# Kernel tuning notes

Measured on AMD Instinct MI355X. Metric: run time of the kernel, lower is better.

The kernel has to match this reference:

```python
import jax, jax.numpy as jnp
import numpy as np

NEG_SLOPE = 0.01  # torch LeakyReLU default

def setup_inputs() -> dict:
    key = jax.random.key(0)
    ks = jax.random.split(key, 8)
    B, T, D = 8, 2048, 512
    E, H = 8, 2 * D  # n_experts, ffn hidden
    s = 0.02
    return {
        "x":  jax.random.normal(ks[0], (B, T, D), dtype=jnp.float32),
        "Wr": jax.random.normal(ks[1], (D, E), dtype=jnp.float32) * s,
        "br": jnp.zeros((E,), dtype=jnp.float32),
        "W1": jax.random.normal(ks[2], (E, D, H), dtype=jnp.float32) * s,
        "b1": jnp.zeros((E, H), dtype=jnp.float32),
        "W2": jax.random.normal(ks[3], (E, H, D), dtype=jnp.float32) * s,
        "b2": jnp.zeros((E, D), dtype=jnp.float32),
    }

def reference(x, Wr, br, W1, b1, W2, b2):
    B, T, D = x.shape
    E = Wr.shape[1]
    top_k = 2
    balancing_coef = 1e-4
    x_flat = x.reshape(B * T, D)  # [N, D]

    # router: softmax over experts
    router_probs = jax.nn.softmax(x_flat @ Wr + br, axis=-1)  # [N, E]
    top_weights, top_indices = jax.lax.top_k(router_probs, top_k)  # [N, k]

    # dense all-expert FFN (faithful to original: every expert on every token)
    h = jax.nn.leaky_relu(jnp.einsum('nd,edh->neh', x_flat, W1) + b1, NEG_SLOPE)  # [N, E, H]
    expert_out = jax.nn.leaky_relu(jnp.einsum('neh,ehd->ned', h, W2) + b2, NEG_SLOPE)  # [N, E, D]
    # dropout is identity in eval mode

    # gather top-k expert outputs and combine with router weights
    top_out = jnp.take_along_axis(expert_out, top_indices[:, :, None], axis=1)  # [N, k, D]
    out_flat = jnp.sum(top_out * top_weights[:, :, None], axis=1)  # [N, D]
    output = out_flat.reshape(B, T, D)

    # load-balancing loss
    target = jnp.full((E,), 1.0 / E, dtype=x.dtype)
    mean_probs = jnp.mean(router_probs, axis=0)
    gating_loss = jnp.mean((target - mean_probs) ** 2) * balancing_coef
    return (output, gating_loss)
```

## Files before the change

kernel.cpp:

```cpp
#include <hip/hip_runtime.h>
#include <hip/hip_bf16.h>

constexpr int D_    = 512;
constexpr int H_    = 1024;
constexpr int E_    = 8;
constexpr int NTOK_ = 16384;
constexpr int MT_   = 64;
constexpr int NPAIR_= 2*NTOK_;
constexpr float NEG_ = 0.01f;

typedef short s16x8 __attribute__((ext_vector_type(8)));
typedef float f32x4 __attribute__((ext_vector_type(4)));

#define MFMA16(a,b,c) __builtin_amdgcn_mfma_f32_16x16x32_bf16((a),(b),(c),0,0,0)

__device__ __forceinline__ unsigned short f2bf(float f) {
  unsigned u = __float_as_uint(f);
  u += 0x7FFFu + ((u >> 16) & 1u);
  return (unsigned short)(u >> 16);
}
__device__ __forceinline__ float bf2f(unsigned u16) {
  return __uint_as_float(u16 << 16);
}
__device__ __forceinline__ float leaky(float v) {
  return v > 0.f ? v : NEG_ * v;
}

__global__ __launch_bounds__(256) void router_kernel(
    const float* __restrict__ x, const float* __restrict__ Wr,
    const float* __restrict__ br,
    int* __restrict__ cnt, float* __restrict__ psum,
    int* __restrict__ tokE, int* __restrict__ tokSlot, float* __restrict__ tokW) {
  const int blk = blockIdx.x;
  const int tid = threadIdx.x;
  __shared__ float SH[8256 + 32];
  const int t0 = blk * 64;
  float* xt   = SH;
  float* red  = SH;
  float* lp   = SH + 8256;
  int*  lcnt  = (int*)(SH + 8256 + 8);
  int*  gbase = (int*)(SH + 8256 + 16);
  if (tid < 8) { lcnt[tid] = 0; lp[tid] = 0.f; }

  const int tq = tid & 63;
  const int q  = tid >> 6;
  float acc[E_];
#pragma unroll
  for (int e = 0; e < E_; e++) acc[e] = 0.f;

  for (int c = 0; c < 4; c++) {
    __syncthreads();
#pragma unroll
    for (int it = 0; it < 8; it++) {
      int f = it * 256 + tid;
      int row = f >> 5, c4 = f & 31;
      float4 v = *(const float4*)(x + (size_t)(t0 + row) * D_ + c * 128 + c4 * 4);
      float* d = xt + row * 129 + c4 * 4;
      d[0] = v.x; d[1] = v.y; d[2] = v.z; d[3] = v.w;
    }
    __syncthreads();
#pragma unroll
    for (int j = 0; j < 32; j++) {
      float xv = xt[tq * 129 + q * 32 + j];
      const float* wr = Wr + (size_t)(c * 128 + q * 32 + j) * E_;
#pragma unroll
      for (int e = 0; e < E_; e++) acc[e] += xv * wr[e];
    }
  }
  __syncthreads();
#pragma unroll
  for (int e = 0; e < E_; e++) red[(q * 64 + tq) * 8 + e] = acc[e];
  __syncthreads();

  float m1 = -1.f, m2 = -1.f; int i1 = 0, i2 = 0, s1 = 0, s2 = 0;
  if (tid < 64) {
    float p[E_];
#pragma unroll
    for (int e = 0; e < E_; e++)
      p[e] = br[e] + red[tid * 8 + e] + red[(64 + tid) * 8 + e]
           + red[(128 + tid) * 8 + e] + red[(192 + tid) * 8 + e];
    float mx = p[0];
#pragma unroll
    for (int e = 1; e < E_; e++) mx = fmaxf(mx, p[e]);
    float s = 0.f;
#pragma unroll
    for (int e = 0; e < E_; e++) { p[e] = expf(p[e] - mx); s += p[e]; }
    float inv = 1.f / s;
#pragma unroll
    for (int e = 0; e < E_; e++) p[e] *= inv;

#pragma unroll
    for (int e = 0; e < E_; e++) {
      float pe = p[e];
      if (pe > m1)      { m2 = m1; i2 = i1; m1 = pe; i1 = e; }
      else if (pe > m2) { m2 = pe; i2 = e; }
    }
    s1 = atomicAdd(&lcnt[i1], 1);
    s2 = atomicAdd(&lcnt[i2], 1);
#pragma unroll
    for (int e = 0; e < E_; e++) atomicAdd(&lp[e], p[e]);
  }
  __syncthreads();
  if (tid < 8) {
    gbase[tid] = atomicAdd(&cnt[tid * 16], lcnt[tid]);
    atomicAdd(&psum[tid * 16], lp[tid]);
  }
  __syncthreads();
  if (tid < 64) {
    int gt = t0 + tid;
    tokE[2 * gt]     = i1; tokSlot[2 * gt]     = gbase[i1] + s1; tokW[2 * gt]     = m1;
    tokE[2 * gt + 1] = i2; tokSlot[2 * gt + 1] = gbase[i2] + s2; tokW[2 * gt + 1] = m2;
  }
}

__global__ __launch_bounds__(256) void convert_kernel(
    const float* __restrict__ W1, const float* __restrict__ W2,
    unsigned short* __restrict__ W1s, unsigned short* __restrict__ W2s) {
  __shared__ float ldsf[64 * 68];
  const int tid = threadIdx.x;
  int bid = blockIdx.x;
  const float* src;
  int eE, kt, tc, srcStride;
  bool isW1 = bid < 1024;
  if (isW1) {
    eE = bid >> 7; kt = (bid >> 4) & 7; tc = bid & 15; srcStride = 1024;
    src = W1 + ((size_t)(eE * 512 + kt * 64)) * 1024 + tc * 64;
  } else {
    int b2i = bid - 1024;
    eE = b2i >> 7; kt = (b2i >> 3) & 15; tc = b2i & 7; srcStride = 512;
    src = W2 + ((size_t)(eE * 1024 + kt * 64)) * 512 + tc * 64;
  }
#pragma unroll
  for (int rep = 0; rep < 4; rep++) {
    int row = rep * 16 + (tid >> 4);
    int c4  = (tid & 15) * 4;
    float4 v = *(const float4*)(src + (size_t)row * srcStride + c4);
    float* d = ldsf + row * 68 + c4;
    d[0] = v.x; d[1] = v.y; d[2] = v.z; d[3] = v.w;
  }
  __syncthreads();
  int wv = tid >> 6, lane = tid & 63;
#pragma unroll
  for (int qi = 0; qi < 2; qi++) {
    int qq = wv * 2 + qi;
    int ks = qq >> 2, nt = qq & 3;
    int k0 = ks * 32 + (lane >> 4) * 8;
    int n  = nt * 16 + (lane & 15);
    s16x8 v;
#pragma unroll
    for (int j = 0; j < 8; j++) v[j] = (short)f2bf(ldsf[(k0 + j) * 68 + n]);
    int ntg = tc * 4 + nt, kkg = kt * 2 + ks;
    if (isW1)
      *(s16x8*)(W1s + (((size_t)eE << 16) + (ntg << 10) + (kkg << 6) + lane) * 8) = v;
    else
      *(s16x8*)(W2s + (((size_t)eE << 16) + (ntg << 11) + (kkg << 6) + lane) * 8) = v;
  }
}

__global__ __launch_bounds__(256) void assign_kernel(
    const int* __restrict__ tokE, const int* __restrict__ tokSlot,
    const int* __restrict__ cnt, const float* __restrict__ psum,
    int* __restrict__ posOfTok, int* __restrict__ tokOfPos,
    float* __restrict__ loss_out) {
  __shared__ int soff[E_];
  int tid = threadIdx.x;
  if (tid == 0) {
    int o = 0;
#pragma unroll
    for (int e = 0; e < E_; e++) { soff[e] = o; o += cnt[e * 16]; }
  }
  __syncthreads();
  int p = blockIdx.x * 256 + tid;
  int pos = soff[tokE[p]] + tokSlot[p];
  posOfTok[p] = pos;
  tokOfPos[pos] = p >> 1;
  if (blockIdx.x == 0 && tid == 0) {
    float l = 0.f;
#pragma unroll
    for (int e = 0; e < E_; e++) {
      float d = 0.125f - psum[e * 16] / (float)NTOK_;
      l += d * d;
    }
    *loss_out = (l / 8.f) * 1e-4f;
  }
}

__global__ __launch_bounds__(512, 2) void ffn_kernel(
    const float* __restrict__ x,
    const unsigned short* __restrict__ W1s, const unsigned short* __restrict__ W2s,
    const float* __restrict__ b1, const float* __restrict__ b2,
    const int* __restrict__ cnt, const int* __restrict__ tokOfPos,
    unsigned short* __restrict__ buf) {
  const int e = blockIdx.x & 7;
  const int tile = blockIdx.x >> 3;
  int nTok = 0, base0 = 0;
#pragma unroll
  for (int i = 0; i < E_; i++) {
    int ci = cnt[i * 16];
    if (i < e) base0 += ci;
    if (i == e) nTok = ci;
  }
  const int start = tile * MT_;
  if (start >= nTok) return;
  const int valid = min(MT_, nTok - start);
  const int base = base0 + start;

  __shared__ __align__(16) unsigned short L[MT_][1032];

  const int tid = threadIdx.x;
  const int w = tid >> 6;
  const int lane = tid & 63;

  for (int r = w; r < MT_; r += 8) {
    int tok = tokOfPos[base + min(r, valid - 1)];
    const float4* src = (const float4*)(x + (size_t)tok * D_);
    float4 a = src[lane * 2], b = src[lane * 2 + 1];
    s16x8 v;
    v[0] = (short)f2bf(a.x); v[1] = (short)f2bf(a.y);
    v[2] = (short)f2bf(a.z); v[3] = (short)f2bf(a.w);
    v[4] = (short)f2bf(b.x); v[5] = (short)f2bf(b.y);
    v[6] = (short)f2bf(b.z); v[7] = (short)f2bf(b.w);
    *(s16x8*)&L[r][lane * 8] = v;
  }
  __syncthreads();

  const int qm = lane & 15;
  const int qk = (lane >> 4) * 8;
  const int qr = (lane >> 4) * 4;

  const unsigned short* A1 =
      W1s + (((size_t)e << 16) + ((size_t)(w * 8) << 10) + lane) * 8;
  f32x4 acc1[8][4];
#pragma unroll
  for (int mi = 0; mi < 8; mi++)
#pragma unroll
    for (int ni = 0; ni < 4; ni++) acc1[mi][ni] = {0.f, 0.f, 0.f, 0.f};

  s16x8 a1p[2][8];
#pragma unroll
  for (int s = 0; s < 2; s++)
#pragma unroll
    for (int mi = 0; mi < 8; mi++)
      a1p[s][mi] = *(const s16x8*)(A1 + (size_t)mi * 8192 + s * 512);

#pragma unroll
  for (int kk = 0; kk < 16; kk++) {
    s16x8 bcur[4];
#pragma unroll
    for (int ni = 0; ni < 4; ni++)
      bcur[ni] = *(const s16x8*)&L[ni * 16 + qm][kk * 32 + qk];
    __builtin_amdgcn_s_setprio(1);
#pragma unroll
    for (int mi = 0; mi < 8; mi++)
#pragma unroll
      for (int ni = 0; ni < 4; ni++)
        acc1[mi][ni] = MFMA16(a1p[kk & 1][mi], bcur[ni], acc1[mi][ni]);
    __builtin_amdgcn_s_setprio(0);
    if (kk + 2 < 16) {
#pragma unroll
      for (int mi = 0; mi < 8; mi++)
        a1p[kk & 1][mi] = *(const s16x8*)(A1 + (size_t)mi * 8192 + (kk + 2) * 512);
    }
  }
  __syncthreads();

  const unsigned short* A2 =
      W2s + (((size_t)e << 16) + ((size_t)(w * 4) << 11) + lane) * 8;
  s16x8 a2p[2][4];
#pragma unroll
  for (int s = 0; s < 2; s++)
#pragma unroll
    for (int mi = 0; mi < 4; mi++)
      a2p[s][mi] = *(const s16x8*)(A2 + (size_t)mi * 16384 + s * 512);

#pragma unroll
  for (int mi = 0; mi < 8; mi++) {
    int hb = w * 128 + mi * 16 + qr;
    float4 bv = *(const float4*)(b1 + (size_t)e * H_ + hb);
#pragma unroll
    for (int ni = 0; ni < 4; ni++) {
      int tr = ni * 16 + qm;
      ushort4 pk;
      pk.x = f2bf(leaky(acc1[mi][ni][0] + bv.x));
      pk.y = f2bf(leaky(acc1[mi][ni][1] + bv.y));
      pk.z = f2bf(leaky(acc1[mi][ni][2] + bv.z));
      pk.w = f2bf(leaky(acc1[mi][ni][3] + bv.w));
      *(ushort4*)&L[tr][hb] = pk;
    }
  }
  __syncthreads();

  f32x4 acc2[4][4];
#pragma unroll
  for (int mi = 0; mi < 4; mi++)
#pragma unroll
    for (int ni = 0; ni < 4; ni++) acc2[mi][ni] = {0.f, 0.f, 0.f, 0.f};

#pragma unroll
  for (int kk = 0; kk < 32; kk++) {
    s16x8 bcur[4];
#pragma unroll
    for (int ni = 0; ni < 4; ni++)
      bcur[ni] = *(const s16x8*)&L[ni * 16 + qm][kk * 32 + qk];
    __builtin_amdgcn_s_setprio(1);
#pragma unroll
    for (int mi = 0; mi < 4; mi++)
#pragma unroll
      for (int ni = 0; ni < 4; ni++)
        acc2[mi][ni] = MFMA16(a2p[kk & 1][mi], bcur[ni], acc2[mi][ni]);
    __builtin_amdgcn_s_setprio(0);
    if (kk + 2 < 32) {
#pragma unroll
      for (int mi = 0; mi < 4; mi++)
        a2p[kk & 1][mi] = *(const s16x8*)(A2 + (size_t)mi * 16384 + (kk + 2) * 512);
    }
  }

#pragma unroll
  for (int mi = 0; mi < 4; mi++) {
    int ob = w * 64 + mi * 16 + qr;
    float4 bv = *(const float4*)(b2 + (size_t)e * D_ + ob);
#pragma unroll
    for (int ni = 0; ni < 4; ni++) {
      int tok = ni * 16 + qm;
      if (tok < valid) {
        ushort4 pk;
        pk.x = f2bf(leaky(acc2[mi][ni][0] + bv.x));
        pk.y = f2bf(leaky(acc2[mi][ni][1] + bv.y));
        pk.z = f2bf(leaky(acc2[mi][ni][2] + bv.z));
        pk.w = f2bf(leaky(acc2[mi][ni][3] + bv.w));
        *(ushort4*)(buf + (size_t)(base + tok) * D_ + ob) = pk;
      }
    }
  }
}

__global__ __launch_bounds__(256) void combine_kernel(
    const unsigned short* __restrict__ buf, const int* __restrict__ posOfTok,
    const float* __restrict__ tokW, float* __restrict__ out) {
  int t = blockIdx.x * 4 + (threadIdx.x >> 6);
  int lane = threadIdx.x & 63;
  int p0 = posOfTok[2 * t], p1 = posOfTok[2 * t + 1];
  float w0 = tokW[2 * t], w1 = tokW[2 * t + 1];
  uint4 u0 = ((const uint4*)(buf + (size_t)p0 * D_))[lane];
  uint4 u1 = ((const uint4*)(buf + (size_t)p1 * D_))[lane];
  float4 oA, oB;
  oA.x = w0 * bf2f(u0.x & 0xFFFFu) + w1 * bf2f(u1.x & 0xFFFFu);
  oA.y = w0 * bf2f(u0.x >> 16)     + w1 * bf2f(u1.x >> 16);
  oA.z = w0 * bf2f(u0.y & 0xFFFFu) + w1 * bf2f(u1.y & 0xFFFFu);
  oA.w = w0 * bf2f(u0.y >> 16)     + w1 * bf2f(u1.y >> 16);
  oB.x = w0 * bf2f(u0.z & 0xFFFFu) + w1 * bf2f(u1.z & 0xFFFFu);
  oB.y = w0 * bf2f(u0.z >> 16)     + w1 * bf2f(u1.z >> 16);
  oB.z = w0 * bf2f(u0.w & 0xFFFFu) + w1 * bf2f(u1.w & 0xFFFFu);
  oB.w = w0 * bf2f(u0.w >> 16)     + w1 * bf2f(u1.w >> 16);
  float4* dst = (float4*)(out + (size_t)t * D_);
  dst[lane * 2]     = oA;
  dst[lane * 2 + 1] = oB;
}

extern "C" void kernel_launch(void* const* d_in, const int* in_sizes, int n_in,
                              void* d_out, int out_size, void* d_ws, size_t ws_size,
                              hipStream_t stream) {
  const float* x  = (const float*)d_in[0];
  const float* Wr = (const float*)d_in[1];
  const float* br = (const float*)d_in[2];
  const float* W1 = (const float*)d_in[3];
  const float* b1 = (const float*)d_in[4];
  const float* W2 = (const float*)d_in[5];
  const float* b2 = (const float*)d_in[6];
  float* out = (float*)d_out;

  char* ws = (char*)d_ws;
  int*   cnt      = (int*)(ws + 0);
  float* psum     = (float*)(ws + 512);
  int*   tokE     = (int*)(ws + 4096);
  int*   tokSlot  = (int*)(ws + 4096 + 1 * 131072);
  float* tokW     = (float*)(ws + 4096 + 2 * 131072);
  int*   posOfTok = (int*)(ws + 4096 + 3 * 131072);
  int*   tokOfPos = (int*)(ws + 4096 + 4 * 131072);
  unsigned short* W1s = (unsigned short*)(ws + (1u << 20));
  unsigned short* W2s = (unsigned short*)(ws + (1u << 20) + 16777216u);
  unsigned short* buf = (unsigned short*)(ws + (1u << 20) + 33554432u);

  hipMemsetAsync(d_ws, 0, 2048, stream);
  router_kernel<<<256, 256, 0, stream>>>(x, Wr, br, cnt, psum, tokE, tokSlot, tokW);
  convert_kernel<<<2048, 256, 0, stream>>>(W1, W2, W1s, W2s);
  assign_kernel<<<NPAIR_ / 256, 256, 0, stream>>>(tokE, tokSlot, cnt, psum,
                                                  posOfTok, tokOfPos,
                                                  out + (size_t)NTOK_ * D_);
  ffn_kernel<<<(NTOK_ / MT_) * E_, 512, 0, stream>>>(x, W1s, W2s, b1, b2,
                                                     cnt, tokOfPos, buf);
  combine_kernel<<<NTOK_ / 4, 256, 0, stream>>>(buf, posOfTok, tokW, out);
}
```

Baseline: 261.4 us.

## Switch FFN to 32x32x16 MFMA with 1024-thread blocks and new weight swizzle

Replaces the 16x16x32 bf16 MFMA tiles with 32x32x16 MFMA tiles, changes the pre-swizzled weight layout in the convert kernel to match, and doubles the FFN block to 16 waves so each wave owns fewer output rows. Larger MFMA tiles cut the number of LDS B-operand reads per FLOP, and more waves per block aim to hide latency. The cost is fewer accumulators per wave, deeper weight prefetch rings, and launch_bounds(1024,4), which tightens the register budget and may cause spills or lower occupancy given the large LDS tile.

```diff
diff --git a/kernel.cpp b/kernel.cpp
--- a/kernel.cpp
+++ b/kernel.cpp
@@ -9,10 +9,10 @@
 constexpr int NPAIR_= 2*NTOK_;
 constexpr float NEG_ = 0.01f;
 
-typedef short s16x8 __attribute__((ext_vector_type(8)));
-typedef float f32x4 __attribute__((ext_vector_type(4)));
-
-#define MFMA16(a,b,c) __builtin_amdgcn_mfma_f32_16x16x32_bf16((a),(b),(c),0,0,0)
+typedef short s16x8  __attribute__((ext_vector_type(8)));
+typedef float f32x16 __attribute__((ext_vector_type(16)));
+
+#define MFMA32(a,b,c) __builtin_amdgcn_mfma_f32_32x32x16_bf16((a),(b),(c),0,0,0)
 
 __device__ __forceinline__ unsigned short f2bf(float f) {
   unsigned u = __float_as_uint(f);
@@ -140,20 +140,24 @@
   }
   __syncthreads();
   int wv = tid >> 6, lane = tid & 63;
+  int hi = lane >> 5, lm = lane & 31;
 #pragma unroll
   for (int qi = 0; qi < 2; qi++) {
     int qq = wv * 2 + qi;
-    int ks = qq >> 2, nt = qq & 3;
-    int k0 = ks * 32 + (lane >> 4) * 8;
-    int n  = nt * 16 + (lane & 15);
+    int ksl = qq >> 1;
+    int ntl = qq & 1;
+    int k0  = ksl * 16 + hi * 8;
+    int n   = ntl * 32 + lm;
     s16x8 v;
 #pragma unroll
     for (int j = 0; j < 8; j++) v[j] = (short)f2bf(ldsf[(k0 + j) * 68 + n]);
-    int ntg = tc * 4 + nt, kkg = kt * 2 + ks;
-    if (isW1)
-      *(s16x8*)(W1s + (((size_t)eE << 16) + (ntg << 10) + (kkg << 6) + lane) * 8) = v;
-    else
-      *(s16x8*)(W2s + (((size_t)eE << 16) + (ntg << 11) + (kkg << 6) + lane) * 8) = v;
+    if (isW1) {
+      int nt = tc * 2 + ntl, ks = kt * 4 + ksl;
+      *(s16x8*)(W1s + (size_t)eE * 524288 + nt * 16384 + ks * 512 + lane * 8) = v;
+    } else {
+      int nt = tc * 2 + ntl, ks = kt * 4 + ksl;
+      *(s16x8*)(W2s + (size_t)eE * 524288 + nt * 32768 + ks * 512 + lane * 8) = v;
+    }
   }
 }
 
@@ -185,7 +189,7 @@
   }
 }
 
-__global__ __launch_bounds__(512, 2) void ffn_kernel(
+__global__ __launch_bounds__(1024, 4) void ffn_kernel(
     const float* __restrict__ x,
     const unsigned short* __restrict__ W1s, const unsigned short* __restrict__ W2s,
     const float* __restrict__ b1, const float* __restrict__ b2,
@@ -210,8 +214,10 @@
   const int tid = threadIdx.x;
   const int w = tid >> 6;
   const int lane = tid & 63;
-
-  for (int r = w; r < MT_; r += 8) {
+  const int tq = lane & 31;
+  const int hi = lane >> 5;
+
+  for (int r = w; r < MT_; r += 16) {
     int tok = tokOfPos[base + min(r, valid - 1)];
     const float4* src = (const float4*)(x + (size_t)tok * D_);
     float4 a = src[lane * 2], b = src[lane * 2 + 1];
@@ -224,112 +230,108 @@
   }
   __syncthreads();
 
-  const int qm = lane & 15;
-  const int qk = (lane >> 4) * 8;
-  const int qr = (lane >> 4) * 4;
-
   const unsigned short* A1 =
-      W1s + (((size_t)e << 16) + ((size_t)(w * 8) << 10) + lane) * 8;
-  f32x4 acc1[8][4];
-#pragma unroll
-  for (int mi = 0; mi < 8; mi++)
-#pragma unroll
-    for (int ni = 0; ni < 4; ni++) acc1[mi][ni] = {0.f, 0.f, 0.f, 0.f};
-
-  s16x8 a1p[2][8];
-#pragma unroll
-  for (int s = 0; s < 2; s++)
-#pragma unroll
-    for (int mi = 0; mi < 8; mi++)
-      a1p[s][mi] = *(const s16x8*)(A1 + (size_t)mi * 8192 + s * 512);
-
-#pragma unroll
-  for (int kk = 0; kk < 16; kk++) {
-    s16x8 bcur[4];
-#pragma unroll
-    for (int ni = 0; ni < 4; ni++)
-      bcur[ni] = *(const s16x8*)&L[ni * 16 + qm][kk * 32 + qk];
+      W1s + (size_t)e * 524288 + (size_t)(w * 2) * 16384 + lane * 8;
+  f32x16 acc1[2][2];
+#pragma unroll
+  for (int mi = 0; mi < 2; mi++)
+#pragma unroll
+    for (int ni = 0; ni < 2; ni++)
+#pragma unroll
+      for (int r = 0; r < 16; r++) acc1[mi][ni][r] = 0.f;
+
+  s16x8 a1p[4][2];
+#pragma unroll
+  for (int s = 0; s < 4; s++)
+#pragma unroll
+    for (int mi = 0; mi < 2; mi++)
+      a1p[s][mi] = *(const s16x8*)(A1 + (size_t)(mi * 32 + s) * 512);
+
+#pragma unroll
+  for (int ks = 0; ks < 32; ks++) {
+    s16x8 bcur[2];
+#pragma unroll
+    for (int ni = 0; ni < 2; ni++)
+      bcur[ni] = *(const s16x8*)&L[ni * 32 + tq][ks * 16 + hi * 8];
     __builtin_amdgcn_s_setprio(1);
 #pragma unroll
-    for (int mi = 0; mi < 8; mi++)
-#pragma unroll
-      for (int ni = 0; ni < 4; ni++)
-        acc1[mi][ni] = MFMA16(a1p[kk & 1][mi], bcur[ni], acc1[mi][ni]);
+    for (int mi = 0; mi < 2; mi++)
+#pragma unroll
+      for (int ni = 0; ni < 2; ni++)
+        acc1[mi][ni] = MFMA32(a1p[ks & 3][mi], bcur[ni], acc1[mi][ni]);
     __builtin_amdgcn_s_setprio(0);
-    if (kk + 2 < 16) {
-#pragma unroll
-      for (int mi = 0; mi < 8; mi++)
-        a1p[kk & 1][mi] = *(const s16x8*)(A1 + (size_t)mi * 8192 + (kk + 2) * 512);
+    if (ks + 4 < 32) {
+#pragma unroll
+      for (int mi = 0; mi < 2; mi++)
+        a1p[ks & 3][mi] = *(const s16x8*)(A1 + (size_t)(mi * 32 + ks + 4) * 512);
     }
   }
   __syncthreads();
 
   const unsigned short* A2 =
-      W2s + (((size_t)e << 16) + ((size_t)(w * 4) << 11) + lane) * 8;
-  s16x8 a2p[2][4];
-#pragma unroll
-  for (int s = 0; s < 2; s++)
-#pragma unroll
-    for (int mi = 0; mi < 4; mi++)
-      a2p[s][mi] = *(const s16x8*)(A2 + (size_t)mi * 16384 + s * 512);
-
-#pragma unroll
-  for (int mi = 0; mi < 8; mi++) {
-    int hb = w * 128 + mi * 16 + qr;
-    float4 bv = *(const float4*)(b1 + (size_t)e * H_ + hb);
-#pragma unroll
-    for (int ni = 0; ni < 4; ni++) {
-      int tr = ni * 16 + qm;
-      ushort4 pk;
-      pk.x = f2bf(leaky(acc1[mi][ni][0] + bv.x));
-      pk.y = f2bf(leaky(acc1[mi][ni][1] + bv.y));
-      pk.z = f2bf(leaky(acc1[mi][ni][2] + bv.z));
-      pk.w = f2bf(leaky(acc1[mi][ni][3] + bv.w));
-      *(ushort4*)&L[tr][hb] = pk;
-    }
-  }
-  __syncthreads();
-
-  f32x4 acc2[4][4];
-#pragma unroll
-  for (int mi = 0; mi < 4; mi++)
-#pragma unroll
-    for (int ni = 0; ni < 4; ni++) acc2[mi][ni] = {0.f, 0.f, 0.f, 0.f};
-
-#pragma unroll
-  for (int kk = 0; kk < 32; kk++) {
-    s16x8 bcur[4];
-#pragma unroll
-    for (int ni = 0; ni < 4; ni++)
-      bcur[ni] = *(const s16x8*)&L[ni * 16 + qm][kk * 32 + qk];
+      W2s + (size_t)e * 524288 + (size_t)w * 32768 + lane * 8;
+  s16x8 a2p[8];
+#pragma unroll
+  for (int s = 0; s < 8; s++)
+    a2p[s] = *(const s16x8*)(A2 + (size_t)s * 512);
+
+#pragma unroll
+  for (int mi = 0; mi < 2; mi++) {
+#pragma unroll
+    for (int g = 0; g < 4; g++) {
+      int hb = w * 64 + mi * 32 + g * 8 + hi * 4;
+      float4 bv = *(const float4*)(b1 + (size_t)e * H_ + hb);
+#pragma unroll
+      for (int ni = 0; ni < 2; ni++) {
+        int tr = ni * 32 + tq;
+        ushort4 pk;
+        pk.x = f2bf(leaky(acc1[mi][ni][g * 4 + 0] + bv.x));
+        pk.y = f2bf(leaky(acc1[mi][ni][g * 4 + 1] + bv.y));
+        pk.z = f2bf(leaky(acc1[mi][ni][g * 4 + 2] + bv.z));
+        pk.w = f2bf(leaky(acc1[mi][ni][g * 4 + 3] + bv.w));
+        *(ushort4*)&L[tr][hb] = pk;
+      }
+    }
+  }
+  __syncthreads();
+
+  f32x16 acc2[2];
+#pragma unroll
+  for (int ni = 0; ni < 2; ni++)
+#pragma unroll
+    for (int r = 0; r < 16; r++) acc2[ni][r] = 0.f;
+
+#pragma unroll
+  for (int ks = 0; ks < 64; ks++) {
+    s16x8 bcur[2];
+#pragma unroll
+    for (int ni = 0; ni < 2; ni++)
+      bcur[ni] = *(const s16x8*)&L[ni * 32 + tq][ks * 16 + hi * 8];
     __builtin_amdgcn_s_setprio(1);
 #pragma unroll
-    for (int mi = 0; mi < 4; mi++)
-#pragma unroll
-      for (int ni = 0; ni < 4; ni++)
-        acc2[mi][ni] = MFMA16(a2p[kk & 1][mi], bcur[ni], acc2[mi][ni]);
+    for (int ni = 0; ni < 2; ni++)
+      acc2[ni] = MFMA32(a2p[ks & 7], bcur[ni], acc2[ni]);
     __builtin_amdgcn_s_setprio(0);
-    if (kk + 2 < 32) {
-#pragma unroll
-      for (int mi = 0; mi < 4; mi++)
-        a2p[kk & 1][mi] = *(const s16x8*)(A2 + (size_t)mi * 16384 + (kk + 2) * 512);
-    }
-  }
-
-#pragma unroll
-  for (int mi = 0; mi < 4; mi++) {
-    int ob = w * 64 + mi * 16 + qr;
-    float4 bv = *(const float4*)(b2 + (size_t)e * D_ + ob);
-#pragma unroll
-    for (int ni = 0; ni < 4; ni++) {
-      int tok = ni * 16 + qm;
-      if (tok < valid) {
+    if (ks + 8 < 64) {
+      a2p[ks & 7] = *(const s16x8*)(A2 + (size_t)(ks + 8) * 512);
+    }
+  }
+
+#pragma unroll
+  for (int ni = 0; ni < 2; ni++) {
+    int tok = ni * 32 + tq;
+    if (tok < valid) {
+      size_t rowbase = (size_t)(base + tok) * D_;
+#pragma unroll
+      for (int g = 0; g < 4; g++) {
+        int ob = w * 32 + g * 8 + hi * 4;
+        float4 bv = *(const float4*)(b2 + (size_t)e * D_ + ob);
         ushort4 pk;
-        pk.x = f2bf(leaky(acc2[mi][ni][0] + bv.x));
-        pk.y = f2bf(leaky(acc2[mi][ni][1] + bv.y));
-        pk.z = f2bf(leaky(acc2[mi][ni][2] + bv.z));
-        pk.w = f2bf(leaky(acc2[mi][ni][3] + bv.w));
-        *(ushort4*)(buf + (size_t)(base + tok) * D_ + ob) = pk;
+        pk.x = f2bf(leaky(acc2[ni][g * 4 + 0] + bv.x));
+        pk.y = f2bf(leaky(acc2[ni][g * 4 + 1] + bv.y));
+        pk.z = f2bf(leaky(acc2[ni][g * 4 + 2] + bv.z));
+        pk.w = f2bf(leaky(acc2[ni][g * 4 + 3] + bv.w));
+        *(ushort4*)(buf + rowbase + ob) = pk;
       }
     }
   }
@@ -388,7 +390,7 @@
   assign_kernel<<<NPAIR_ / 256, 256, 0, stream>>>(tokE, tokSlot, cnt, psum,
                                                   posOfTok, tokOfPos,
                                                   out + (size_t)NTOK_ * D_);
-  ffn_kernel<<<(NTOK_ / MT_) * E_, 512, 0, stream>>>(x, W1s, W2s, b1, b2,
-                                                     cnt, tokOfPos, buf);
+  ffn_kernel<<<(NTOK_ / MT_) * E_, 1024, 0, stream>>>(x, W1s, W2s, b1, b2,
+                                                      cnt, tokOfPos, buf);
   combine_kernel<<<NTOK_ / 4, 256, 0, stream>>>(buf, posOfTok, tokW, out);
 }
```

After: 277.1 us. 6.0% more time.

## Merge router and weight conversion into one launch and drop assign kernel

Applied to the files above, without the earlier changes.

Router and weight-conversion blocks now run in a single prep kernel, with block ranges picking the role. The router also writes per-expert token lists directly, indexed by expert and slot, so the separate assign pass goes away. Combine recomputes each pair's position from the expert offsets and tokE/tokSlot, and computes the gating loss itself. This removes two kernel launches and a global round-trip. In exchange the tokOfPosE array grows to E×NTOK entries and the prep blocks carry the larger shared-memory footprint.

```diff
diff --git a/kernel.cpp b/kernel.cpp
--- a/kernel.cpp
+++ b/kernel.cpp
@@ -6,7 +6,6 @@
 constexpr int E_    = 8;
 constexpr int NTOK_ = 16384;
 constexpr int MT_   = 64;
-constexpr int NPAIR_= 2*NTOK_;
 constexpr float NEG_ = 0.01f;
 
 typedef short s16x8 __attribute__((ext_vector_type(8)));
@@ -26,162 +25,137 @@
   return v > 0.f ? v : NEG_ * v;
 }
 
-__global__ __launch_bounds__(256) void router_kernel(
+__global__ __launch_bounds__(256) void prep_kernel(
     const float* __restrict__ x, const float* __restrict__ Wr,
     const float* __restrict__ br,
+    const float* __restrict__ W1, const float* __restrict__ W2,
+    unsigned short* __restrict__ W1s, unsigned short* __restrict__ W2s,
     int* __restrict__ cnt, float* __restrict__ psum,
-    int* __restrict__ tokE, int* __restrict__ tokSlot, float* __restrict__ tokW) {
+    int* __restrict__ tokE, int* __restrict__ tokSlot, float* __restrict__ tokW,
+    int* __restrict__ tokOfPosE) {
   const int blk = blockIdx.x;
   const int tid = threadIdx.x;
   __shared__ float SH[8256 + 32];
-  const int t0 = blk * 64;
-  float* xt   = SH;
-  float* red  = SH;
-  float* lp   = SH + 8256;
-  int*  lcnt  = (int*)(SH + 8256 + 8);
-  int*  gbase = (int*)(SH + 8256 + 16);
-  if (tid < 8) { lcnt[tid] = 0; lp[tid] = 0.f; }
-
-  const int tq = tid & 63;
-  const int q  = tid >> 6;
-  float acc[E_];
-#pragma unroll
-  for (int e = 0; e < E_; e++) acc[e] = 0.f;
-
-  for (int c = 0; c < 4; c++) {
-    __syncthreads();
-#pragma unroll
-    for (int it = 0; it < 8; it++) {
-      int f = it * 256 + tid;
-      int row = f >> 5, c4 = f & 31;
-      float4 v = *(const float4*)(x + (size_t)(t0 + row) * D_ + c * 128 + c4 * 4);
-      float* d = xt + row * 129 + c4 * 4;
+  if (blk < 256) {
+    const int t0 = blk * 64;
+    float* xt   = SH;
+    float* red  = SH;
+    float* lp   = SH + 8256;
+    int*  lcnt  = (int*)(SH + 8256 + 8);
+    int*  gbase = (int*)(SH + 8256 + 16);
+    if (tid < 8) { lcnt[tid] = 0; lp[tid] = 0.f; }
+
+    const int tq = tid & 63;
+    const int q  = tid >> 6;
+    float acc[E_];
+#pragma unroll
+    for (int e = 0; e < E_; e++) acc[e] = 0.f;
+
+    for (int c = 0; c < 4; c++) {
+      __syncthreads();
+#pragma unroll
+      for (int it = 0; it < 8; it++) {
+        int f = it * 256 + tid;
+        int row = f >> 5, c4 = f & 31;
+        float4 v = *(const float4*)(x + (size_t)(t0 + row) * D_ + c * 128 + c4 * 4);
+        float* d = xt + row * 129 + c4 * 4;
+        d[0] = v.x; d[1] = v.y; d[2] = v.z; d[3] = v.w;
+      }
+      __syncthreads();
+#pragma unroll
+      for (int j = 0; j < 32; j++) {
+        float xv = xt[tq * 129 + q * 32 + j];
+        const float* wr = Wr + (size_t)(c * 128 + q * 32 + j) * E_;
+#pragma unroll
+        for (int e = 0; e < E_; e++) acc[e] += xv * wr[e];
+      }
+    }
+    __syncthreads();
+#pragma unroll
+    for (int e = 0; e < E_; e++) red[(q * 64 + tq) * 8 + e] = acc[e];
+    __syncthreads();
+
+    float m1 = -1.f, m2 = -1.f; int i1 = 0, i2 = 0, s1 = 0, s2 = 0;
+    if (tid < 64) {
+      float p[E_];
+#pragma unroll
+      for (int e = 0; e < E_; e++)
+        p[e] = br[e] + red[tid * 8 + e] + red[(64 + tid) * 8 + e]
+             + red[(128 + tid) * 8 + e] + red[(192 + tid) * 8 + e];
+      float mx = p[0];
+#pragma unroll
+      for (int e = 1; e < E_; e++) mx = fmaxf(mx, p[e]);
+      float s = 0.f;
+#pragma unroll
+      for (int e = 0; e < E_; e++) { p[e] = expf(p[e] - mx); s += p[e]; }
+      float inv = 1.f / s;
+#pragma unroll
+      for (int e = 0; e < E_; e++) p[e] *= inv;
+
+#pragma unroll
+      for (int e = 0; e < E_; e++) {
+        float pe = p[e];
+        if (pe > m1)      { m2 = m1; i2 = i1; m1 = pe; i1 = e; }
+        else if (pe > m2) { m2 = pe; i2 = e; }
+      }
+      s1 = atomicAdd(&lcnt[i1], 1);
+      s2 = atomicAdd(&lcnt[i2], 1);
+#pragma unroll
+      for (int e = 0; e < E_; e++) atomicAdd(&lp[e], p[e]);
+    }
+    __syncthreads();
+    if (tid < 8) {
+      gbase[tid] = atomicAdd(&cnt[tid * 16], lcnt[tid]);
+      atomicAdd(&psum[tid * 16], lp[tid]);
+    }
+    __syncthreads();
+    if (tid < 64) {
+      int gt = t0 + tid;
+      int sl1 = gbase[i1] + s1, sl2 = gbase[i2] + s2;
+      tokE[2 * gt]     = i1; tokSlot[2 * gt]     = sl1; tokW[2 * gt]     = m1;
+      tokE[2 * gt + 1] = i2; tokSlot[2 * gt + 1] = sl2; tokW[2 * gt + 1] = m2;
+      tokOfPosE[i1 * NTOK_ + sl1] = gt;
+      tokOfPosE[i2 * NTOK_ + sl2] = gt;
+    }
+  } else {
+    float* ldsf = SH;
+    int bid = blk - 256;
+    const float* src;
+    int eE, kt, tc, srcStride;
+    bool isW1 = bid < 1024;
+    if (isW1) {
+      eE = bid >> 7; kt = (bid >> 4) & 7; tc = bid & 15; srcStride = 1024;
+      src = W1 + ((size_t)(eE * 512 + kt * 64)) * 1024 + tc * 64;
+    } else {
+      int b2i = bid - 1024;
+      eE = b2i >> 7; kt = (b2i >> 3) & 15; tc = b2i & 7; srcStride = 512;
+      src = W2 + ((size_t)(eE * 1024 + kt * 64)) * 512 + tc * 64;
+    }
+#pragma unroll
+    for (int rep = 0; rep < 4; rep++) {
+      int row = rep * 16 + (tid >> 4);
+      int c4  = (tid & 15) * 4;
+      float4 v = *(const float4*)(src + (size_t)row * srcStride + c4);
+      float* d = ldsf + row * 68 + c4;
       d[0] = v.x; d[1] = v.y; d[2] = v.z; d[3] = v.w;
     }
     __syncthreads();
-#pragma unroll
-    for (int j = 0; j < 32; j++) {
-      float xv = xt[tq * 129 + q * 32 + j];
-      const float* wr = Wr + (size_t)(c * 128 + q * 32 + j) * E_;
-#pragma unroll
-      for (int e = 0; e < E_; e++) acc[e] += xv * wr[e];
-    }
-  }
-  __syncthreads();
-#pragma unroll
-  for (int e = 0; e < E_; e++) red[(q * 64 + tq) * 8 + e] = acc[e];
-  __syncthreads();
-
-  float m1 = -1.f, m2 = -1.f; int i1 = 0, i2 = 0, s1 = 0, s2 = 0;
-  if (tid < 64) {
-    float p[E_];
-#pragma unroll
-    for (int e = 0; e < E_; e++)
-      p[e] = br[e] + red[tid * 8 + e] + red[(64 + tid) * 8 + e]
-           + red[(128 + tid) * 8 + e] + red[(192 + tid) * 8 + e];
-    float mx = p[0];
-#pragma unroll
-    for (int e = 1; e < E_; e++) mx = fmaxf(mx, p[e]);
-    float s = 0.f;
-#pragma unroll
-    for (int e = 0; e < E_; e++) { p[e] = expf(p[e] - mx); s += p[e]; }
-    float inv = 1.f / s;
-#pragma unroll
-    for (int e = 0; e < E_; e++) p[e] *= inv;
-
-#pragma unroll
-    for (int e = 0; e < E_; e++) {
-      float pe = p[e];
-      if (pe > m1)      { m2 = m1; i2 = i1; m1 = pe; i1 = e; }
-      else if (pe > m2) { m2 = pe; i2 = e; }
-    }
-    s1 = atomicAdd(&lcnt[i1], 1);
-    s2 = atomicAdd(&lcnt[i2], 1);
-#pragma unroll
-    for (int e = 0; e < E_; e++) atomicAdd(&lp[e], p[e]);
-  }
-  __syncthreads();
-  if (tid < 8) {
-    gbase[tid] = atomicAdd(&cnt[tid * 16], lcnt[tid]);
-    atomicAdd(&psum[tid * 16], lp[tid]);
-  }
-  __syncthreads();
-  if (tid < 64) {
-    int gt = t0 + tid;
-    tokE[2 * gt]     = i1; tokSlot[2 * gt]     = gbase[i1] + s1; tokW[2 * gt]     = m1;
-    tokE[2 * gt + 1] = i2; tokSlot[2 * gt + 1] = gbase[i2] + s2; tokW[2 * gt + 1] = m2;
-  }
-}
-
-__global__ __launch_bounds__(256) void convert_kernel(
-    const float* __restrict__ W1, const float* __restrict__ W2,
-    unsigned short* __restrict__ W1s, unsigned short* __restrict__ W2s) {
-  __shared__ float ldsf[64 * 68];
-  const int tid = threadIdx.x;
-  int bid = blockIdx.x;
-  const float* src;
-  int eE, kt, tc, srcStride;
-  bool isW1 = bid < 1024;
-  if (isW1) {
-    eE = bid >> 7; kt = (bid >> 4) & 7; tc = bid & 15; srcStride = 1024;
-    src = W1 + ((size_t)(eE * 512 + kt * 64)) * 1024 + tc * 64;
-  } else {
-    int b2i = bid - 1024;
-    eE = b2i >> 7; kt = (b2i >> 3) & 15; tc = b2i & 7; srcStride = 512;
-    src = W2 + ((size_t)(eE * 1024 + kt * 64)) * 512 + tc * 64;
-  }
-#pragma unroll
-  for (int rep = 0; rep < 4; rep++) {
-    int row = rep * 16 + (tid >> 4);
-    int c4  = (tid & 15) * 4;
-    float4 v = *(const float4*)(src + (size_t)row * srcStride + c4);
-    float* d = ldsf + row * 68 + c4;
-    d[0] = v.x; d[1] = v.y; d[2] = v.z; d[3] = v.w;
-  }
-  __syncthreads();
-  int wv = tid >> 6, lane = tid & 63;
-#pragma unroll
-  for (int qi = 0; qi < 2; qi++) {
-    int qq = wv * 2 + qi;
-    int ks = qq >> 2, nt = qq & 3;
-    int k0 = ks * 32 + (lane >> 4) * 8;
-    int n  = nt * 16 + (lane & 15);
-    s16x8 v;
-#pragma unroll
-    for (int j = 0; j < 8; j++) v[j] = (short)f2bf(ldsf[(k0 + j) * 68 + n]);
-    int ntg = tc * 4 + nt, kkg = kt * 2 + ks;
-    if (isW1)
-      *(s16x8*)(W1s + (((size_t)eE << 16) + (ntg << 10) + (kkg << 6) + lane) * 8) = v;
-    else
-      *(s16x8*)(W2s + (((size_t)eE << 16) + (ntg << 11) + (kkg << 6) + lane) * 8) = v;
-  }
-}
-
-__global__ __launch_bounds__(256) void assign_kernel(
-    const int* __restrict__ tokE, const int* __restrict__ tokSlot,
-    const int* __restrict__ cnt, const float* __restrict__ psum,
-    int* __restrict__ posOfTok, int* __restrict__ tokOfPos,
-    float* __restrict__ loss_out) {
-  __shared__ int soff[E_];
-  int tid = threadIdx.x;
-  if (tid == 0) {
-    int o = 0;
-#pragma unroll
-    for (int e = 0; e < E_; e++) { soff[e] = o; o += cnt[e * 16]; }
-  }
-  __syncthreads();
-  int p = blockIdx.x * 256 + tid;
-  int pos = soff[tokE[p]] + tokSlot[p];
-  posOfTok[p] = pos;
-  tokOfPos[pos] = p >> 1;
-  if (blockIdx.x == 0 && tid == 0) {
-    float l = 0.f;
-#pragma unroll
-    for (int e = 0; e < E_; e++) {
-      float d = 0.125f - psum[e * 16] / (float)NTOK_;
-      l += d * d;
-    }
-    *loss_out = (l / 8.f) * 1e-4f;
+    int wv = tid >> 6, lane = tid & 63;
+#pragma unroll
+    for (int qi = 0; qi < 2; qi++) {
+      int qq = wv * 2 + qi;
+      int ks = qq >> 2, nt = qq & 3;
+      int k0 = ks * 32 + (lane >> 4) * 8;
+      int n  = nt * 16 + (lane & 15);
+      s16x8 v;
+#pragma unroll
+      for (int j = 0; j < 8; j++) v[j] = (short)f2bf(ldsf[(k0 + j) * 68 + n]);
+      int ntg = tc * 4 + nt, kkg = kt * 2 + ks;
+      if (isW1)
+        *(s16x8*)(W1s + (((size_t)eE << 16) + (ntg << 10) + (kkg << 6) + lane) * 8) = v;
+      else
+        *(s16x8*)(W2s + (((size_t)eE << 16) + (ntg << 11) + (kkg << 6) + lane) * 8) = v;
+    }
   }
 }
 
@@ -189,7 +163,7 @@
     const float* __restrict__ x,
     const unsigned short* __restrict__ W1s, const unsigned short* __restrict__ W2s,
     const float* __restrict__ b1, const float* __restrict__ b2,
-    const int* __restrict__ cnt, const int* __restrict__ tokOfPos,
+    const int* __restrict__ cnt, const int* __restrict__ tokOfPosE,
     unsigned short* __restrict__ buf) {
   const int e = blockIdx.x & 7;
   const int tile = blockIdx.x >> 3;
@@ -212,7 +186,7 @@
   const int lane = tid & 63;
 
   for (int r = w; r < MT_; r += 8) {
-    int tok = tokOfPos[base + min(r, valid - 1)];
+    int tok = tokOfPosE[e * NTOK_ + start + min(r, valid - 1)];
     const float4* src = (const float4*)(x + (size_t)tok * D_);
     float4 a = src[lane * 2], b = src[lane * 2 + 1];
     s16x8 v;
@@ -336,11 +310,31 @@
 }
 
 __global__ __launch_bounds__(256) void combine_kernel(
-    const unsigned short* __restrict__ buf, const int* __restrict__ posOfTok,
-    const float* __restrict__ tokW, float* __restrict__ out) {
+    const unsigned short* __restrict__ buf,
+    const int* __restrict__ tokE, const int* __restrict__ tokSlot,
+    const float* __restrict__ tokW,
+    const int* __restrict__ cnt, const float* __restrict__ psum,
+    float* __restrict__ out, float* __restrict__ loss_out) {
+  __shared__ int soff[E_];
+  if (threadIdx.x == 0) {
+    int o = 0;
+#pragma unroll
+    for (int e = 0; e < E_; e++) { soff[e] = o; o += cnt[e * 16]; }
+  }
+  __syncthreads();
+  if (blockIdx.x == 0 && threadIdx.x == 0) {
+    float l = 0.f;
+#pragma unroll
+    for (int e = 0; e < E_; e++) {
+      float d = 0.125f - psum[e * 16] / (float)NTOK_;
+      l += d * d;
+    }
+    *loss_out = (l / 8.f) * 1e-4f;
+  }
   int t = blockIdx.x * 4 + (threadIdx.x >> 6);
   int lane = threadIdx.x & 63;
-  int p0 = posOfTok[2 * t], p1 = posOfTok[2 * t + 1];
+  int p0 = soff[tokE[2 * t]]     + tokSlot[2 * t];
+  int p1 = soff[tokE[2 * t + 1]] + tokSlot[2 * t + 1];
   float w0 = tokW[2 * t], w1 = tokW[2 * t + 1];
   uint4 u0 = ((const uint4*)(buf + (size_t)p0 * D_))[lane];
   uint4 u1 = ((const uint4*)(buf + (size_t)p1 * D_))[lane];
@@ -376,19 +370,18 @@
   int*   tokE     = (int*)(ws + 4096);
   int*   tokSlot  = (int*)(ws + 4096 + 1 * 131072);
   float* tokW     = (float*)(ws + 4096 + 2 * 131072);
-  int*   posOfTok = (int*)(ws + 4096 + 3 * 131072);
-  int*   tokOfPos = (int*)(ws + 4096 + 4 * 131072);
+  int*   tokOfPosE= (int*)(ws + 4096 + 3 * 131072);
   unsigned short* W1s = (unsigned short*)(ws + (1u << 20));
   unsigned short* W2s = (unsigned short*)(ws + (1u << 20) + 16777216u);
   unsigned short* buf = (unsigned short*)(ws + (1u << 20) + 33554432u);
 
   hipMemsetAsync(d_ws, 0, 2048, stream);
-  router_kernel<<<256, 256, 0, stream>>>(x, Wr, br, cnt, psum, tokE, tokSlot, tokW);
-  convert_kernel<<<2048, 256, 0, stream>>>(W1, W2, W1s, W2s);
-  assign_kernel<<<NPAIR_ / 256, 256, 0, stream>>>(tokE, tokSlot, cnt, psum,
-                                                  posOfTok, tokOfPos,
-                                                  out + (size_t)NTOK_ * D_);
+  prep_kernel<<<256 + 2048, 256, 0, stream>>>(x, Wr, br, W1, W2, W1s, W2s,
+                                              cnt, psum, tokE, tokSlot, tokW,
+                                              tokOfPosE);
   ffn_kernel<<<(NTOK_ / MT_) * E_, 512, 0, stream>>>(x, W1s, W2s, b1, b2,
-                                                     cnt, tokOfPos, buf);
-  combine_kernel<<<NTOK_ / 4, 256, 0, stream>>>(buf, posOfTok, tokW, out);
-}
+                                                     cnt, tokOfPosE, buf);
+  combine_kernel<<<NTOK_ / 4, 256, 0, stream>>>(buf, tokE, tokSlot, tokW,
+                                                cnt, psum, out,
+                                                out + (size_t)NTOK_ * D_);
+}
```

After: 258.9 us. About the same (-0.9%).
